# Optimization experiments

Measured on AMD Instinct MI355X. Metric: run time of the kernel, lower is better.

## Reference

```python
import jax, jax.numpy as jnp
import numpy as np

EPS = 1e-6
POS_THR, NEG_THR = 0.5, 0.4
ALPHA, GAMMA = 0.25, 2.0
CAND_THR = 0.3  # per-target candidate IoU threshold
TOPK_PER_TARGET = 3
NEG_RATIO_CAP = 3


def _make_boxes(key, shape, wh_lo, wh_hi):
    # valid x1y1x2y2 boxes in [0,1] coords
    k1, k2 = jax.random.split(key)
    xy1 = jax.random.uniform(k1, shape[:-1] + (2,)) * 0.8
    wh = jax.random.uniform(k2, shape[:-1] + (2,)) * (wh_hi - wh_lo) + wh_lo
    return jnp.concatenate([xy1, xy1 + wh], axis=-1).astype(jnp.float32)


def setup_inputs() -> dict:
    key = jax.random.key(0)
    B, A, T = 16, 65536, 32
    k1, k2, k3, k4 = jax.random.split(key, 4)
    bbox_pred = _make_boxes(k1, (B, A, 4), 0.05, 0.30)
    conf_pred = jax.random.uniform(k2, (B, A), minval=1e-4, maxval=1 - 1e-4).astype(jnp.float32)
    anchors = _make_boxes(k3, (A, 4), 0.05, 0.30)
    target_boxes = _make_boxes(k4, (B, T, 4), 0.10, 0.35)
    return {"bbox_pred": bbox_pred, "conf_pred": conf_pred, "anchors": anchors,
            "target_boxes": target_boxes}


def _box_iou(b1, b2):
    # b1: [A,4], b2: [T,4] -> [A,T]
    x1 = jnp.maximum(b1[:, None, 0], b2[None, :, 0])
    y1 = jnp.maximum(b1[:, None, 1], b2[None, :, 1])
    x2 = jnp.minimum(b1[:, None, 2], b2[None, :, 2])
    y2 = jnp.minimum(b1[:, None, 3], b2[None, :, 3])
    inter = jnp.clip(x2 - x1, 0) * jnp.clip(y2 - y1, 0)
    area1 = (b1[:, 2] - b1[:, 0]) * (b1[:, 3] - b1[:, 1])
    area2 = (b2[:, 2] - b2[:, 0]) * (b2[:, 3] - b2[:, 1])
    union = area1[:, None] + area2[None, :] - inter
    return inter / (union + EPS)


def _giou_loss(b1, b2):
    # b1, b2: [P,4] -> [P]
    x1 = jnp.maximum(b1[:, 0], b2[:, 0]); y1 = jnp.maximum(b1[:, 1], b2[:, 1])
    x2 = jnp.minimum(b1[:, 2], b2[:, 2]); y2 = jnp.minimum(b1[:, 3], b2[:, 3])
    inter = jnp.clip(x2 - x1, 0) * jnp.clip(y2 - y1, 0)
    area1 = (b1[:, 2] - b1[:, 0]) * (b1[:, 3] - b1[:, 1])
    area2 = (b2[:, 2] - b2[:, 0]) * (b2[:, 3] - b2[:, 1])
    union = area1 + area2 - inter
    iou = inter / (union + EPS)
    ex1 = jnp.minimum(b1[:, 0], b2[:, 0]); ey1 = jnp.minimum(b1[:, 1], b2[:, 1])
    ex2 = jnp.maximum(b1[:, 2], b2[:, 2]); ey2 = jnp.maximum(b1[:, 3], b2[:, 3])
    enc = (ex2 - ex1) * (ey2 - ey1)
    giou = iou - (enc - union) / (enc + EPS)
    return 1.0 - giou


def _per_image(bbox_p, conf_p, anchors, tboxes):
    # bbox_p: [A,4], conf_p: [A], anchors: [A,4], tboxes: [T,4]
    A = anchors.shape[0]
    ious = _box_iou(anchors, tboxes)                   # [A,T]
    max_ious = ious.max(axis=1)
    best_t = ious.argmax(axis=1)                       # [A]

    # per-target forced positives: top-k (k=min(3,#cand), at least argmax) over ALL anchors
    top_vals, top_idx = jax.lax.top_k(ious.T, TOPK_PER_TARGET)  # [T,3]
    num_cand = (ious > CAND_THR).sum(axis=0)                    # [T]
    k_t = jnp.maximum(1, jnp.minimum(TOPK_PER_TARGET, num_cand))
    take = jnp.arange(TOPK_PER_TARGET)[None, :] < k_t[:, None]  # [T,3]
    forced = jnp.zeros((A,), bool).at[top_idx.reshape(-1)].max(take.reshape(-1))

    pos = (max_ious >= POS_THR) | forced
    neg = (max_ious < NEG_THR) & (~pos)

    # focal loss (scores are probabilities; no sigmoid, matching the original)
    pt = jnp.where(pos, conf_p, 1.0 - conf_p)
    alpha_f = jnp.where(pos, ALPHA, 1.0 - ALPHA)
    focal = -alpha_f * (1.0 - pt) ** GAMMA * jnp.log(jnp.clip(pt, EPS, 1.0 - EPS))

    # hard-negative mining: keep top max_neg negatives by focal loss.
    # (forced positives guarantee num_pos >= 1, so the num_pos==0 branch is dead)
    num_pos = pos.sum()
    neg_ratio = jnp.minimum(NEG_RATIO_CAP, A // num_pos)
    max_neg = neg_ratio * num_pos
    neg_scores = jnp.where(neg, focal, -jnp.inf)
    order = jnp.argsort(-neg_scores)
    rank = jnp.zeros((A,), jnp.int32).at[order].set(jnp.arange(A, dtype=jnp.int32))
    sel_neg = neg & (rank < max_neg)  # if #neg <= max_neg this keeps all negatives
    loss_mask = pos | sel_neg
    conf_loss = jnp.sum(jnp.where(loss_mask, focal, 0.0)) / jnp.maximum(loss_mask.sum(), 1)

    # bbox loss over positives: GIoU + 0.5 * mean-L1 against matched target
    matched = tboxes[best_t]                           # [A,4]
    per_anchor = _giou_loss(bbox_p, matched) + 0.5 * jnp.abs(bbox_p - matched).mean(axis=1)
    posf = pos.astype(bbox_p.dtype)
    bbox_loss = jnp.sum(per_anchor * posf) / jnp.maximum(num_pos, 1)
    return conf_loss, bbox_loss


def reference(bbox_pred, conf_pred, anchors, target_boxes):
    conf_l, bbox_l = jax.vmap(_per_image, in_axes=(0, 0, None, 0))(
        bbox_pred, conf_pred, anchors, target_boxes)
    conf_weight, bbox_weight = 1.0, 1.0
    total = conf_weight * conf_l.mean() + bbox_weight * bbox_l.mean()
    return total
```

## Files before the change

kernel.cpp:

```cpp
#include <hip/hip_runtime.h>
#include <math.h>

#define EPSF 1e-6f
#define ACH 1024
#define NBIN 1024
#define CAPB 64
#define BIASU 0x4000000000000000ull

struct Part { unsigned long long q0, q1, q2, cand; };

__device__ __forceinline__ double u2d(unsigned long long x){return __longlong_as_double((long long)x);}
__device__ __forceinline__ unsigned long long d2u(double x){return (unsigned long long)__double_as_longlong(x);}

__device__ __forceinline__ void ins3d(double p, double &q0, double &q1, double &q2) {
  double n0 = fmax(q0,p), x = fmin(q0,p);
  double n1 = fmax(q1,x), y = fmin(q1,x);
  double n2 = fmax(q2,y);
  q0=n0; q1=n1; q2=n2;
}

__device__ __forceinline__ float focal_neg(float c) {
  float pt = 1.f - c;
  float ptc = fminf(fmaxf(pt, EPSF), 1.f - EPSF);
  float om = 1.f - pt;
  return -0.75f * om * om * logf(ptc);
}

__global__ __launch_bounds__(256, 4) void k_fused(
    const float4* __restrict__ anchors, const float4* __restrict__ tboxes,
    const float* __restrict__ conf_pred, const float4* __restrict__ bbox_pred,
    Part* __restrict__ parts, unsigned* __restrict__ ghsC, float* __restrict__ ghsF,
    float* __restrict__ accPosP, float* __restrict__ accBboxP,
    unsigned* __restrict__ cntPosP, unsigned* __restrict__ cntNegP,
    float* __restrict__ out, int A, int T, int nch) {
  __shared__ unsigned long long buf[32][CAPB+1];
  __shared__ unsigned cnt[32];
  __shared__ float4 st[32];
  __shared__ unsigned h[NBIN];
  __shared__ float hf[NBIN];
  __shared__ float sP[256], sB[256];
  __shared__ int cP[256], cN[256];
  int chunk = blockIdx.x, b = blockIdx.y;
  int tid = threadIdx.x;
  int base = chunk * ACH;
  if (tid < 32) cnt[tid] = 0;
  if (tid < T) st[tid] = tboxes[b*T + tid];
  for (int i = tid; i < NBIN; i += 256) { h[i] = 0; hf[i] = 0.f; }
  if (chunk == 4 && b == 0 && tid == 0) out[0] = 0.f;
  int i0 = base + tid;
  float4 a0 = anchors[i0], a1 = anchors[i0+256], a2 = anchors[i0+512], a3 = anchors[i0+768];
  float ar0=(a0.z-a0.x)*(a0.w-a0.y), ar1=(a1.z-a1.x)*(a1.w-a1.y);
  float ar2=(a2.z-a2.x)*(a2.w-a2.y), ar3=(a3.z-a3.x)*(a3.w-a3.y);
  __syncthreads();
  float bn0=-1.f,bd0=1.f, bn1=-1.f,bd1=1.f, bn2=-1.f,bd2=1.f, bn3=-1.f,bd3=1.f;
  int bt0=0, bt1=0, bt2=0, bt3=0;

#define PROC(av, arv, bnv, bdv, btv, idxv) { \
    float ix1=fmaxf(av.x,tv.x), iy1=fmaxf(av.y,tv.y); \
    float ix2=fminf(av.z,tv.z), iy2=fminf(av.w,tv.w); \
    float inter=fmaxf(ix2-ix1,0.f)*fmaxf(iy2-iy1,0.f); \
    float sa = arv + ta; \
    float u = sa - inter, d = u + EPSF;            \
    bool gt = inter*bdv > bnv*d;                   \
    bnv=gt?inter:bnv; bdv=gt?d:bdv; btv=gt?tt:btv; \
    if (__builtin_expect(inter > 0.3f*d, 0)) {     \
      float iou = inter * __builtin_amdgcn_rcpf(d); \
      unsigned slot = atomicAdd(&cnt[tt], 1u); \
      if (slot < CAPB) \
        buf[tt][slot] = ((unsigned long long)__float_as_uint(iou)<<32) \
                      | (unsigned long long)(0xFFFFFFFFu-(unsigned)(idxv)) | BIASU; \
    } \
  }

  #pragma unroll 4
  for (int tt = 0; tt < T; ++tt) {
    float4 tv = tboxes[b*T + tt];
    float ta = (tv.z-tv.x)*(tv.w-tv.y);
    PROC(a0, ar0, bn0, bd0, bt0, i0)
    PROC(a1, ar1, bn1, bd1, bt1, i0+256)
    PROC(a2, ar2, bn2, bd2, bt2, i0+512)
    PROC(a3, ar3, bn3, bd3, bt3, i0+768)
  }
#undef PROC

  size_t gb = (size_t)b * A;
  float fsum=0.f, bsum=0.f; int cpos=0, cneg=0;
#define EPI(bnv, bdv, btv, idxv) { \
    float mi = bnv/bdv;                      \
    size_t ia = gb + (size_t)(idxv); \
    float conf = conf_pred[ia]; \
    bool isPos = mi >= 0.5f; \
    bool isNeg = mi < 0.4f; \
    if (isNeg) { \
      int bin = min(NBIN-1,(int)(conf*1024.f)); \
      atomicAdd(&h[bin],1u); \
      atomicAdd(&hf[bin], focal_neg(conf)); \
      cneg++; \
    } \
    if (isPos) { \
      cpos++; \
      float ptc = fminf(fmaxf(conf, EPSF), 1.f-EPSF); \
      float om = 1.f - conf; \
      fsum += -0.25f * om * om * logf(ptc); \
      float4 pb = bbox_pred[ia]; float4 m = st[btv]; \
      float ix1=fmaxf(pb.x,m.x), iy1=fmaxf(pb.y,m.y); \
      float ix2=fminf(pb.z,m.z), iy2=fminf(pb.w,m.w); \
      float inter=fmaxf(ix2-ix1,0.f)*fmaxf(iy2-iy1,0.f); \
      float aa1=(pb.z-pb.x)*(pb.w-pb.y); \
      float aa2=(m.z-m.x)*(m.w-m.y); \
      float uni = aa1 + aa2 - inter; \
      float iou = inter/(uni+EPSF); \
      float ex1=fminf(pb.x,m.x), ey1=fminf(pb.y,m.y); \
      float ex2=fmaxf(pb.z,m.z), ey2=fmaxf(pb.w,m.w); \
      float enc=(ex2-ex1)*(ey2-ey1); \
      float giou = iou - (enc-uni)/(enc+EPSF); \
      float l1 = fabsf(pb.x-m.x)+fabsf(pb.y-m.y)+fabsf(pb.z-m.z)+fabsf(pb.w-m.w); \
      bsum += (1.f - giou) + 0.125f*l1; \
    } \
  }
  EPI(bn0, bd0, bt0, i0)
  EPI(bn1, bd1, bt1, i0+256)
  EPI(bn2, bd2, bt2, i0+512)
  EPI(bn3, bd3, bt3, i0+768)
#undef EPI

  sP[tid]=fsum; sB[tid]=bsum; cP[tid]=cpos; cN[tid]=cneg;
  __syncthreads();
  for (int s=128;s>0;s>>=1) {
    if (tid<s){ sP[tid]+=sP[tid+s]; sB[tid]+=sB[tid+s]; cP[tid]+=cP[tid+s]; cN[tid]+=cN[tid+s]; }
    __syncthreads();
  }
  if (tid == 0) {
    int pidx = b*nch + chunk;
    accPosP[pidx]  = sP[0];
    accBboxP[pidx] = sB[0];
    cntPosP[pidx]  = (unsigned)cP[0];
    cntNegP[pidx]  = (unsigned)cN[0];
  }
  for (int i = tid; i < NBIN; i += 256) {
    ghsC[(size_t)(b*nch + chunk)*NBIN + i] = h[i];
    ghsF[(size_t)(b*nch + chunk)*NBIN + i] = hf[i];
  }

  const double BIASD = u2d(BIASU);
  if (tid < 32 && tid < T) {
    unsigned n = cnt[tid];
    if (n <= CAPB) {
      double q0=BIASD, q1=BIASD, q2=BIASD;
      for (unsigned j = 0; j < n; ++j) ins3d(u2d(buf[tid][j]), q0,q1,q2);
      Part p; p.q0=d2u(q0); p.q1=d2u(q1); p.q2=d2u(q2); p.cand=n;
      parts[(b*T+tid)*nch+chunk] = p;
    }
  }
  if (tid < 64) {
    unsigned long long ovf = __ballot(tid < T && cnt[tid] > CAPB);
    while (ovf) {
      int t = __ffsll(ovf) - 1;
      ovf &= ovf - 1;
      float4 tv = tboxes[b*T + t];
      float ta = (tv.z-tv.x)*(tv.w-tv.y);
      double q0=BIASD, q1=BIASD, q2=BIASD;
      for (int j = 0; j < ACH; j += 64) {
        int idx = base + j + tid;
        float4 an = anchors[idx];
        float aa = (an.z-an.x)*(an.w-an.y);
        float ix1=fmaxf(an.x,tv.x), iy1=fmaxf(an.y,tv.y);
        float ix2=fminf(an.z,tv.z), iy2=fminf(an.w,tv.w);
        float inter=fmaxf(ix2-ix1,0.f)*fmaxf(iy2-iy1,0.f);
        float d = (aa+ta)-inter + EPSF;
        if (inter > 0.3f*d) {
          float iou = inter / d;
          unsigned long long pk = ((unsigned long long)__float_as_uint(iou)<<32)
                                | (unsigned long long)(0xFFFFFFFFu-(unsigned)idx) | BIASU;
          ins3d(u2d(pk), q0,q1,q2);
        }
      }
      for (int s=1;s<64;s<<=1) {
        double r0=__shfl_xor(q0,s,64), r1=__shfl_xor(q1,s,64), r2=__shfl_xor(q2,s,64);
        ins3d(r0,q0,q1,q2); ins3d(r1,q0,q1,q2); ins3d(r2,q0,q1,q2);
      }
      if (tid == 0) {
        Part p; p.q0=d2u(q0); p.q1=d2u(q1); p.q2=d2u(q2); p.cand=cnt[t];
        parts[(b*T+t)*nch+chunk] = p;
      }
    }
  }
}

__global__ __launch_bounds__(1024) void k_tail(
    const float4* __restrict__ anchors, const float4* __restrict__ tboxes,
    const Part* __restrict__ parts,
    const float* __restrict__ conf_pred, const float4* __restrict__ bbox_pred,
    const unsigned* __restrict__ ghsC, const float* __restrict__ ghsF,
    const float* __restrict__ accPosP, const float* __restrict__ accBboxP,
    const unsigned* __restrict__ cntPosP, const unsigned* __restrict__ cntNegP,
    float* __restrict__ out, int A, int T, int nch, int B) {
  __shared__ double s0[1024], s1[1024], s2[1024];
  __shared__ unsigned scnt[1024];
  __shared__ unsigned hhC[NBIN];
  __shared__ float hhF[NBIN];
  __shared__ unsigned sc[NBIN];
  __shared__ float sredf[1024];
  __shared__ float4 st[32];
  __shared__ int flist[160];
  __shared__ unsigned fcnt;
  __shared__ float corrP, corrB;
  __shared__ unsigned corrNP, corrNN;
  __shared__ float accPos_s, accBbox_s;
  __shared__ unsigned cntPos_s, cntNeg_s;
  __shared__ int sSelB, sKrem;
  int b = blockIdx.x, tid = threadIdx.x;
  const double BIASD = u2d(BIASU);
  if (tid < T) st[tid] = tboxes[b*T + tid];
  if (tid == 0) { fcnt = 0; corrP = 0.f; corrB = 0.f; corrNP = 0u; corrNN = 0u; }
  __syncthreads();

  {
    int t = tid & 31, g = tid >> 5;
    double q0=BIASD, q1=BIASD, q2=BIASD;
    unsigned long long cand = 0;
    if (t < T) {
      const Part* pp = parts + (size_t)(b*T + t)*nch;
      for (int c = g; c < nch; c += 32) {
        Part p = pp[c];
        ins3d(u2d(p.q0),q0,q1,q2); ins3d(u2d(p.q1),q0,q1,q2); ins3d(u2d(p.q2),q0,q1,q2);
        cand += p.cand;
      }
    }
    s0[tid]=q0; s1[tid]=q1; s2[tid]=q2; scnt[tid]=(unsigned)cand;
    __syncthreads();
    for (int s=512; s>=32; s>>=1) {
      if (tid < s) {
        double a0=s0[tid], a1=s1[tid], a2=s2[tid];
        ins3d(s0[tid+s],a0,a1,a2); ins3d(s1[tid+s],a0,a1,a2); ins3d(s2[tid+s],a0,a1,a2);
        s0[tid]=a0; s1[tid]=a1; s2[tid]=a2; scnt[tid]+=scnt[tid+s];
      }
      __syncthreads();
    }
    if (tid < 32 && tid < T) {
      unsigned cd = scnt[tid];
      if (cd > 0) {
        int kt = cd > 3 ? 3 : (int)cd;
        unsigned long long tp[3] = {d2u(s0[tid]), d2u(s1[tid]), d2u(s2[tid])};
        for (int j = 0; j < kt; ++j) {
          int idx = (int)(0xFFFFFFFFu - (unsigned)(tp[j] & 0xFFFFFFFFull));
          flist[atomicAdd(&fcnt, 1u)] = idx;
        }
      }
    }
    __syncthreads();
  }
  for (int t2 = 0; t2 < T; ++t2) {
    if (scnt[t2] == 0) {
      float4 tv = st[t2];
      float ta = (tv.z-tv.x)*(tv.w-tv.y);
      double m = BIASD;
      for (int a = tid; a < A; a += 1024) {
        float4 an = anchors[a];
        float aa = (an.z-an.x)*(an.w-an.y);
        float ix1=fmaxf(an.x,tv.x), iy1=fmaxf(an.y,tv.y);
        float ix2=fminf(an.z,tv.z), iy2=fminf(an.w,tv.w);
        float inter=fmaxf(ix2-ix1,0.f)*fmaxf(iy2-iy1,0.f);
        float iou = inter / ((aa+ta)-inter + EPSF);
        unsigned long long pk = ((unsigned long long)__float_as_uint(iou)<<32)
                              | (unsigned long long)(0xFFFFFFFFu-(unsigned)a) | BIASU;
        m = fmax(m, u2d(pk));
      }
      s0[tid] = m;
      __syncthreads();
      for (int s=512;s>0;s>>=1) { if (tid<s) s0[tid]=fmax(s0[tid],s0[tid+s]); __syncthreads(); }
      if (tid == 0) {
        int idx = (int)(0xFFFFFFFFu - (unsigned)(d2u(s0[0]) & 0xFFFFFFFFull));
        flist[atomicAdd(&fcnt, 1u)] = idx;
      }
      __syncthreads();
    }
  }
  {
    unsigned accC = 0; float accF = 0.f;
    const unsigned* bc = ghsC + (size_t)b*nch*NBIN + tid;
    const float*    bf = ghsF + (size_t)b*nch*NBIN + tid;
    #pragma unroll 16
    for (int c = 0; c < 64; ++c) {
      accC += bc[(size_t)c*NBIN];
      accF += bf[(size_t)c*NBIN];
    }
    hhC[tid] = accC; hhF[tid] = accF;
  }
  __syncthreads();
  {
    unsigned n = min(fcnt, 160u);
    size_t gb = (size_t)b * A;
    for (unsigned i = tid; i < n; i += 1024) {
      int idx = flist[i];
      bool dup = false;
      for (unsigned j = 0; j < i; ++j) if (flist[j] == idx) { dup = true; break; }
      if (dup) continue;
      float4 an = anchors[idx];
      float ar = (an.z-an.x)*(an.w-an.y);
      float bn=-1.f, bd=1.f; int bt=0;
      for (int tt = 0; tt < T; ++tt) {
        float4 tv = st[tt];
        float ta = (tv.z-tv.x)*(tv.w-tv.y);
        float ix1=fmaxf(an.x,tv.x), iy1=fmaxf(an.y,tv.y);
        float ix2=fminf(an.z,tv.z), iy2=fminf(an.w,tv.w);
        float inter=fmaxf(ix2-ix1,0.f)*fmaxf(iy2-iy1,0.f);
        float u=(ar+ta)-inter, d=u+EPSF;
        bool gt = inter*bd > bn*d;
        bn=gt?inter:bn; bd=gt?d:bd; bt=gt?tt:bt;
      }
      float mi = bn/bd;
      if (mi < 0.5f) {
        size_t ia = gb + (size_t)idx;
        float conf = conf_pred[ia];
        float ptc = fminf(fmaxf(conf, EPSF), 1.f-EPSF);
        float om = 1.f - conf;
        atomicAdd(&corrP, -0.25f*om*om*logf(ptc));
        atomicAdd(&corrNP, 1u);
        float4 pb = bbox_pred[ia]; float4 m = st[bt];
        float ix1=fmaxf(pb.x,m.x), iy1=fmaxf(pb.y,m.y);
        float ix2=fminf(pb.z,m.z), iy2=fminf(pb.w,m.w);
        float inter=fmaxf(ix2-ix1,0.f)*fmaxf(iy2-iy1,0.f);
        float aa1=(pb.z-pb.x)*(pb.w-pb.y);
        float aa2=(m.z-m.x)*(m.w-m.y);
        float uni = aa1 + aa2 - inter;
        float iou = inter/(uni+EPSF);
        float ex1=fminf(pb.x,m.x), ey1=fminf(pb.y,m.y);
        float ex2=fmaxf(pb.z,m.z), ey2=fmaxf(pb.w,m.w);
        float enc=(ex2-ex1)*(ey2-ey1);
        float giou = iou - (enc-uni)/(enc+EPSF);
        float l1 = fabsf(pb.x-m.x)+fabsf(pb.y-m.y)+fabsf(pb.z-m.z)+fabsf(pb.w-m.w);
        atomicAdd(&corrB, (1.f - giou) + 0.125f*l1);
        if (mi < 0.4f) {
          int bin = min(NBIN-1, (int)(conf*1024.f));
          atomicSub(&hhC[bin], 1u);
          atomicAdd(&hhF[bin], -focal_neg(conf));
          atomicAdd(&corrNN, 1u);
        }
      }
    }
  }
  __syncthreads();
  if (tid < 64) {
    float ap = 0.f, ab = 0.f; unsigned np = 0, nn = 0;
    if (tid < nch) {
      int pidx = b*nch + tid;
      ap = accPosP[pidx]; ab = accBboxP[pidx];
      np = cntPosP[pidx]; nn = cntNegP[pidx];
    }
    for (int s = 1; s < 64; s <<= 1) {
      ap += __shfl_xor(ap, s, 64); ab += __shfl_xor(ab, s, 64);
      np += __shfl_xor(np, s, 64); nn += __shfl_xor(nn, s, 64);
    }
    if (tid == 0) {
      accPos_s  = ap + corrP;
      accBbox_s = ab + corrB;
      cntPos_s  = np + corrNP;
      cntNeg_s  = nn - corrNN;
    }
  }
  __syncthreads();
  int np = (int)cntPos_s, nn = (int)cntNeg_s;
  int ratio = (np>0) ? min(3, A/np) : 0;
  int k = min(ratio*np, nn);
  float negSum = 0.f;
  if (k > 0) {
    sc[tid] = hhC[NBIN-1-tid];
    __syncthreads();
    for (int off=1; off<NBIN; off<<=1) {
      unsigned v = (tid >= off) ? sc[tid-off] : 0u;
      __syncthreads();
      sc[tid] += v;
      __syncthreads();
    }
    {
      unsigned Sb  = sc[NBIN-1-tid];
      unsigned Snx = (tid == NBIN-1) ? 0u : sc[NBIN-2-tid];
      if (Sb >= (unsigned)k && Snx < (unsigned)k) { sSelB = tid; sKrem = k - (int)Snx; }
    }
    __syncthreads();
    int selB = sSelB, krem = sKrem;
    sredf[tid] = (tid > selB) ? hhF[tid] : 0.f;
    __syncthreads();
    for (int s=512;s>0;s>>=1){ if(tid<s) sredf[tid]+=sredf[tid+s]; __syncthreads(); }
    float cutMean = hhF[selB] / (float)max(hhC[selB], 1u);
    negSum = sredf[0] + (float)krem * cutMean;
  }
  if (tid==0) {
    float confL = (accPos_s + negSum) / (float)max(np + k, 1);
    float bboxL = accBbox_s / (float)(np > 0 ? np : 1);
    atomicAdd(out, (confL + bboxL) / (float)B);
  }
}

extern "C" void kernel_launch(void* const* d_in, const int* in_sizes, int n_in,
                              void* d_out, int out_size, void* d_ws, size_t ws_size,
                              hipStream_t stream) {
  const float4* bbox_pred = (const float4*)d_in[0];
  const float*  conf_pred = (const float*)d_in[1];
  const float4* anchors   = (const float4*)d_in[2];
  const float4* tboxes    = (const float4*)d_in[3];
  float* out = (float*)d_out;

  int A = in_sizes[2] / 4;
  int B = in_sizes[1] / A;
  int T = in_sizes[3] / (4 * B);
  int nch = A / ACH;
  size_t BA = (size_t)B * A;
  (void)BA;

  Part* parts = (Part*)d_ws;
  unsigned* ghsC = (unsigned*)(parts + (size_t)B*T*nch);
  float* ghsF = (float*)(ghsC + (size_t)B*nch*NBIN);
  float* accPosP  = (float*)(ghsF + (size_t)B*nch*NBIN);
  float* accBboxP = accPosP + (size_t)B*nch;
  unsigned* cntPosP = (unsigned*)(accBboxP + (size_t)B*nch);
  unsigned* cntNegP = cntPosP + (size_t)B*nch;

  dim3 gf((unsigned)nch, (unsigned)B);
  k_fused<<<gf, 256, 0, stream>>>(anchors, tboxes, conf_pred, bbox_pred,
                                  parts, ghsC, ghsF,
                                  accPosP, accBboxP, cntPosP, cntNegP, out, A, T, nch);

  k_tail<<<B, 1024, 0, stream>>>(anchors, tboxes, parts, conf_pred, bbox_pred,
                                 ghsC, ghsF, accPosP, accBboxP, cntPosP, cntNegP,
                                 out, A, T, nch, B);
}
```

Baseline: 68.86 us.

## Replace argmax IoU tracking with threshold margins and deferred candidate bitmask

The inner anchor×target loop no longer tracks the best IoU ratio and target index, and no longer does atomic candidate insertion. It keeps two running max margins (inter - thr·denom) for the 0.4 and 0.5 thresholds, plus a bitmask of targets passing the 0.3 candidate test. Candidate IoUs are computed and buffered in the epilogue by walking the bitmask, and the argmax target is recomputed only for positive anchors. This shortens the hot loop and removes divergent atomics from it, at the cost of redundant IoU recomputation for positives and candidates. Margin comparisons can differ slightly from the divided-ratio comparisons at the threshold boundaries.

```diff
diff --git a/kernel.cpp b/kernel.cpp
--- a/kernel.cpp
+++ b/kernel.cpp
@@ -52,57 +52,77 @@
   float ar0=(a0.z-a0.x)*(a0.w-a0.y), ar1=(a1.z-a1.x)*(a1.w-a1.y);
   float ar2=(a2.z-a2.x)*(a2.w-a2.y), ar3=(a3.z-a3.x)*(a3.w-a3.y);
   __syncthreads();
-  float bn0=-1.f,bd0=1.f, bn1=-1.f,bd1=1.f, bn2=-1.f,bd2=1.f, bn3=-1.f,bd3=1.f;
-  int bt0=0, bt1=0, bt2=0, bt3=0;
-
-#define PROC(av, arv, bnv, bdv, btv, idxv) { \
+  float m04_0=-1.f, m05_0=-1.f, m04_1=-1.f, m05_1=-1.f;
+  float m04_2=-1.f, m05_2=-1.f, m04_3=-1.f, m05_3=-1.f;
+  unsigned cm0=0u, cm1=0u, cm2=0u, cm3=0u;
+
+#define PROC(av, arv, m04v, m05v, cmv) { \
     float ix1=fmaxf(av.x,tv.x), iy1=fmaxf(av.y,tv.y); \
     float ix2=fminf(av.z,tv.z), iy2=fminf(av.w,tv.w); \
     float inter=fmaxf(ix2-ix1,0.f)*fmaxf(iy2-iy1,0.f); \
-    float sa = arv + ta; \
-    float u = sa - inter, d = u + EPSF;            \
-    bool gt = inter*bdv > bnv*d;                   \
-    bnv=gt?inter:bnv; bdv=gt?d:bdv; btv=gt?tt:btv; \
-    if (__builtin_expect(inter > 0.3f*d, 0)) {     \
-      float iou = inter * __builtin_amdgcn_rcpf(d); \
-      unsigned slot = atomicAdd(&cnt[tt], 1u); \
-      if (slot < CAPB) \
-        buf[tt][slot] = ((unsigned long long)__float_as_uint(iou)<<32) \
-                      | (unsigned long long)(0xFFFFFFFFu-(unsigned)(idxv)) | BIASU; \
-    } \
+    float u = (arv + ta) - inter, d = u + EPSF;     \
+    m04v = fmaxf(m04v, fmaf(-0.4f, d, inter)); \
+    m05v = fmaxf(m05v, fmaf(-0.5f, d, inter)); \
+    cmv |= (inter > 0.3f*d) ? bit : 0u; \
   }
 
   #pragma unroll 4
   for (int tt = 0; tt < T; ++tt) {
     float4 tv = tboxes[b*T + tt];
     float ta = (tv.z-tv.x)*(tv.w-tv.y);
-    PROC(a0, ar0, bn0, bd0, bt0, i0)
-    PROC(a1, ar1, bn1, bd1, bt1, i0+256)
-    PROC(a2, ar2, bn2, bd2, bt2, i0+512)
-    PROC(a3, ar3, bn3, bd3, bt3, i0+768)
+    unsigned bit = 1u << tt;
+    PROC(a0, ar0, m04_0, m05_0, cm0)
+    PROC(a1, ar1, m04_1, m05_1, cm1)
+    PROC(a2, ar2, m04_2, m05_2, cm2)
+    PROC(a3, ar3, m04_3, m05_3, cm3)
   }
 #undef PROC
 
   size_t gb = (size_t)b * A;
   float fsum=0.f, bsum=0.f; int cpos=0, cneg=0;
-#define EPI(bnv, bdv, btv, idxv) { \
-    float mi = bnv/bdv;                      \
+#define EPI(av, arv, m04v, m05v, cmv, idxv) { \
     size_t ia = gb + (size_t)(idxv); \
     float conf = conf_pred[ia]; \
-    bool isPos = mi >= 0.5f; \
-    bool isNeg = mi < 0.4f; \
+    bool isPos = m05v >= 0.f; \
+    bool isNeg = m04v < 0.f; \
     if (isNeg) { \
       int bin = min(NBIN-1,(int)(conf*1024.f)); \
       atomicAdd(&h[bin],1u); \
       atomicAdd(&hf[bin], focal_neg(conf)); \
       cneg++; \
     } \
-    if (isPos) { \
+    unsigned cm = cmv; \
+    while (cm) {                            \
+      int tt = __ffs(cm) - 1; cm &= cm - 1; \
+      float4 tv = st[tt]; \
+      float ta = (tv.z-tv.x)*(tv.w-tv.y); \
+      float ix1=fmaxf(av.x,tv.x), iy1=fmaxf(av.y,tv.y); \
+      float ix2=fminf(av.z,tv.z), iy2=fminf(av.w,tv.w); \
+      float inter=fmaxf(ix2-ix1,0.f)*fmaxf(iy2-iy1,0.f); \
+      float d = (arv + ta) - inter + EPSF; \
+      float iou = inter * __builtin_amdgcn_rcpf(d);    \
+      unsigned slot = atomicAdd(&cnt[tt], 1u); \
+      if (slot < CAPB) \
+        buf[tt][slot] = ((unsigned long long)__float_as_uint(iou)<<32) \
+                      | (unsigned long long)(0xFFFFFFFFu-(unsigned)(idxv)) | BIASU; \
+    } \
+    if (isPos) {                            \
       cpos++; \
+      float bn=-1.f, bd=1.f; int bt=0; \
+      for (int tt = 0; tt < T; ++tt) { \
+        float4 tv = st[tt]; \
+        float ta = (tv.z-tv.x)*(tv.w-tv.y); \
+        float ix1=fmaxf(av.x,tv.x), iy1=fmaxf(av.y,tv.y); \
+        float ix2=fminf(av.z,tv.z), iy2=fminf(av.w,tv.w); \
+        float inter=fmaxf(ix2-ix1,0.f)*fmaxf(iy2-iy1,0.f); \
+        float u=(arv+ta)-inter, d=u+EPSF; \
+        bool gt = inter*bd > bn*d;          \
+        bn=gt?inter:bn; bd=gt?d:bd; bt=gt?tt:bt; \
+      } \
       float ptc = fminf(fmaxf(conf, EPSF), 1.f-EPSF); \
       float om = 1.f - conf; \
       fsum += -0.25f * om * om * logf(ptc); \
-      float4 pb = bbox_pred[ia]; float4 m = st[btv]; \
+      float4 pb = bbox_pred[ia]; float4 m = st[bt]; \
       float ix1=fmaxf(pb.x,m.x), iy1=fmaxf(pb.y,m.y); \
       float ix2=fminf(pb.z,m.z), iy2=fminf(pb.w,m.w); \
       float inter=fmaxf(ix2-ix1,0.f)*fmaxf(iy2-iy1,0.f); \
@@ -118,10 +138,10 @@
       bsum += (1.f - giou) + 0.125f*l1; \
     } \
   }
-  EPI(bn0, bd0, bt0, i0)
-  EPI(bn1, bd1, bt1, i0+256)
-  EPI(bn2, bd2, bt2, i0+512)
-  EPI(bn3, bd3, bt3, i0+768)
+  EPI(a0, ar0, m04_0, m05_0, cm0, i0)
+  EPI(a1, ar1, m04_1, m05_1, cm1, i0+256)
+  EPI(a2, ar2, m04_2, m05_2, cm2, i0+512)
+  EPI(a3, ar3, m04_3, m05_3, cm3, i0+768)
 #undef EPI
 
   sP[tid]=fsum; sB[tid]=bsum; cP[tid]=cpos; cN[tid]=cneg;
@@ -298,6 +318,7 @@
       if (dup) continue;
       float4 an = anchors[idx];
       float ar = (an.z-an.x)*(an.w-an.y);
+      float m04=-1.f, m05=-1.f;
       float bn=-1.f, bd=1.f; int bt=0;
       for (int tt = 0; tt < T; ++tt) {
         float4 tv = st[tt];
@@ -306,11 +327,12 @@
         float ix2=fminf(an.z,tv.z), iy2=fminf(an.w,tv.w);
         float inter=fmaxf(ix2-ix1,0.f)*fmaxf(iy2-iy1,0.f);
         float u=(ar+ta)-inter, d=u+EPSF;
+        m04 = fmaxf(m04, fmaf(-0.4f, d, inter));
+        m05 = fmaxf(m05, fmaf(-0.5f, d, inter));
         bool gt = inter*bd > bn*d;
         bn=gt?inter:bn; bd=gt?d:bd; bt=gt?tt:bt;
       }
-      float mi = bn/bd;
-      if (mi < 0.5f) {
+      if (m05 < 0.f) {
         size_t ia = gb + (size_t)idx;
         float conf = conf_pred[ia];
         float ptc = fminf(fmaxf(conf, EPSF), 1.f-EPSF);
@@ -331,7 +353,7 @@
         float giou = iou - (enc-uni)/(enc+EPSF);
         float l1 = fabsf(pb.x-m.x)+fabsf(pb.y-m.y)+fabsf(pb.z-m.z)+fabsf(pb.w-m.w);
         atomicAdd(&corrB, (1.f - giou) + 0.125f*l1);
-        if (mi < 0.4f) {
+        if (m04 < 0.f) {
           int bin = min(NBIN-1, (int)(conf*1024.f));
           atomicSub(&hhC[bin], 1u);
           atomicAdd(&hhF[bin], -focal_neg(conf));
@@ -406,8 +428,6 @@
   int B = in_sizes[1] / A;
   int T = in_sizes[3] / (4 * B);
   int nch = A / ACH;
-  size_t BA = (size_t)B * A;
-  (void)BA;
 
   Part* parts = (Part*)d_ws;
   unsigned* ghsC = (unsigned*)(parts + (size_t)B*T*nch);
```

Result: slower. 79.94 us (+16.1%).
